# Optimization experiments

Measured on AMD Instinct MI355X. Metric: run time of the kernel, lower is better.

Reference implementation:

```python
import jax, jax.numpy as jnp
import numpy as np

C = 100000
D = 512
KEEP_RATIO = 0.5
EPS = 1.1920929e-07  # torch.finfo(float32).eps
K = max(1, int(C * KEEP_RATIO))


def _l2norm(x):
    # F.normalize(dim=-1): x / max(||x||, eps)
    n = jnp.linalg.norm(x, axis=-1, keepdims=True)
    return x / jnp.maximum(n, EPS)


def setup_inputs() -> dict:
    key = jax.random.key(0)
    k1, k2, k3 = jax.random.split(key, 3)
    tensor = jax.random.normal(k1, (1024, D), dtype=jnp.float32)
    target = jax.random.randint(k2, (1024,), 0, C, dtype=jnp.int32)
    # xavier_normal_ on (C, D): std = sqrt(2 / (C + D))
    std = np.sqrt(2.0 / (C + D)).astype(np.float32)
    weight = jax.random.normal(k3, (C, D), dtype=jnp.float32) * std
    return {"tensor": tensor, "target": target, "weight": weight}


def reference(tensor, target, weight):
    # --- target mining (no-grad in original) ---
    t_n = _l2norm(tensor)            # (B, D)
    w_n = _l2norm(weight)            # (C, D)
    # max over batch of cosine similarity -> per-class score (C,)
    scores = jnp.max(jnp.einsum("bd,cd->bc", t_n, w_n), axis=0)
    # ground-truth classes always kept
    scores = scores.at[target].set(2.0)
    _, topk_idx = jax.lax.top_k(scores, K)
    subsample = jnp.sort(topk_idx)                       # (K,) ascending
    # remap targets into subsampled index space (targets guaranteed present)
    new_target = jnp.searchsorted(subsample, target).astype(jnp.int32)
    # --- head ---
    w_sub = weight[subsample]                            # (K, D) gather
    logits = jnp.einsum("bd,kd->bk", _l2norm(tensor), _l2norm(w_sub))
    return logits, new_target
```

## Files before the change

### kernel.cpp

```cpp
#include <hip/hip_runtime.h>

#define C_CLS 100000
#define D_DIM 512
#define B_ROWS 1024
#define K_KEEP 50000
#define EPS_F 1.1920929e-07f
#define MB_CT 64
#define BAND 2e-3f
#define DELTA 4e-4f
#define RMAX 32768

typedef short v8s __attribute__((ext_vector_type(8)));
typedef float v4f __attribute__((ext_vector_type(4)));

struct Ctrl { unsigned prefix; unsigned need; };

__device__ __forceinline__ unsigned key_of(float f){
  unsigned u = __float_as_uint(f);
  return (u & 0x80000000u) ? ~u : (u | 0x80000000u);
}
__device__ __forceinline__ float key_inv(unsigned k){
  unsigned u = (k & 0x80000000u) ? (k & 0x7FFFFFFFu) : ~k;
  return __uint_as_float(u);
}
__device__ __forceinline__ unsigned short f2bf_rne(float f){
  unsigned u = __float_as_uint(f);
  unsigned r = (u + 0x7FFFu + ((u >> 16) & 1u)) >> 16;
  return (unsigned short)r;
}
__device__ __forceinline__ float bf2f(unsigned short h){
  return __uint_as_float(((unsigned)h) << 16);
}


__global__ __launch_bounds__(64) void norm_t_kernel(const float* __restrict__ t, float* __restrict__ tn,
                                                    unsigned short* __restrict__ tnph, unsigned short* __restrict__ tnpl,
                                                    const int* __restrict__ tgt, unsigned* __restrict__ keys){
  int row = blockIdx.x, lane = threadIdx.x;
  if (lane == 0) atomicMax(&keys[tgt[row]], key_of(2.0f));
  const float4* p = (const float4*)(t + (size_t)row * D_DIM);
  float4 a = p[lane*2+0], b = p[lane*2+1];
  float s = a.x*a.x + a.y*a.y + a.z*a.z + a.w*a.w
          + b.x*b.x + b.y*b.y + b.z*b.z + b.w*b.w;
  #pragma unroll
  for (int off = 32; off; off >>= 1) s += __shfl_xor(s, off);
  float den = fmaxf(sqrtf(s), EPS_F);
  float o[8] = {a.x/den, a.y/den, a.z/den, a.w/den, b.x/den, b.y/den, b.z/den, b.w/den};
  float4* q = (float4*)(tn + (size_t)row * D_DIM);
  q[lane*2+0] = make_float4(o[0],o[1],o[2],o[3]);
  q[lane*2+1] = make_float4(o[4],o[5],o[6],o[7]);
  v8s hv, lv;
  #pragma unroll
  for (int j = 0; j < 8; ++j){
    unsigned short h = f2bf_rne(o[j]);
    hv[j] = (short)h;
    lv[j] = (short)f2bf_rne(o[j] - bf2f(h));
  }
  size_t di = (size_t)((row & ~15) + (lane >> 2)) * 512 + (lane & 3) * 128 + (row & 15) * 8;
  *(v8s*)(tnph + di) = hv;
  *(v8s*)(tnpl + di) = lv;
}

__device__ __forceinline__ void load_a2(const unsigned short* __restrict__ tp, int b0, int ks, int lane, v8s* dst){
  #pragma unroll
  for (int i = 0; i < 2; ++i){
    int t = b0 + i*16 + (ks >> 5);
    dst[i] = *(const v8s*)(tp + (size_t)t * 512 + lane * 8);
  }
}

__global__ __launch_bounds__(512, 4) void mine_kernel(
    const unsigned short* __restrict__ tnph, const unsigned short* __restrict__ tnpl,
    const float* __restrict__ w, unsigned* __restrict__ keys,
    float* __restrict__ S, float* __restrict__ winv_g){
  __shared__ unsigned short lw[MB_CT * D_DIM];
  __shared__ float wn[MB_CT];
  const int tid = threadIdx.x;
  const int lane = tid & 63;
  const int cb = blockIdx.x * MB_CT;
  #pragma unroll
  for (int st = 0; st < 8; ++st){
    int g = tid + st * 512;
    int row = g >> 6, fc = g & 63;
    int c = cb + row; if (c >= C_CLS) c = C_CLS - 1;
    const float4* src = (const float4*)(w + (size_t)c * D_DIM + fc * 8);
    float4 v0 = src[0], v1 = src[1];
    float vv[8] = {v0.x,v0.y,v0.z,v0.w,v1.x,v1.y,v1.z,v1.w};
    float s = 0.f;
    #pragma unroll
    for (int j = 0; j < 8; ++j) s += vv[j]*vv[j];
    #pragma unroll
    for (int off = 32; off; off >>= 1) s += __shfl_xor(s, off);
    if (lane == 0) wn[row] = 1.0f / fmaxf(sqrtf(s), EPS_F);
    v8s hv;
    #pragma unroll
    for (int j = 0; j < 8; ++j) hv[j] = (short)f2bf_rne(vv[j]);
    int csw = fc ^ (row & 7);
    *(v8s*)&lw[(size_t)row * D_DIM + csw * 8] = hv;
  }
  __syncthreads();
  if (tid < MB_CT && cb + tid < C_CLS) winv_g[cb + tid] = wn[tid];

  const int wv = tid >> 6;
  const int lr = lane & 15, lg = lane >> 4;
  const int bbase = wv * 128;
  float runmax[4] = {-1e30f,-1e30f,-1e30f,-1e30f};
  v4f acc[4][2];
  #pragma unroll
  for (int j = 0; j < 4; ++j)
    #pragma unroll
    for (int i = 0; i < 2; ++i) acc[j][i] = (v4f){0.f,0.f,0.f,0.f};

  auto mfma_step = [&](int it, v8s* ah, v8s* al){
    const int ks = (it & 15) << 5;
    v8s bh[4];
    #pragma unroll
    for (int j = 0; j < 4; ++j){
      int row = j*16 + lr;
      int ch = ((ks >> 3) + lg) ^ (lr & 7);
      bh[j] = *(const v8s*)&lw[(size_t)row * D_DIM + ch * 8];
    }
    #pragma unroll
    for (int j = 0; j < 4; ++j)
      #pragma unroll
      for (int i = 0; i < 2; ++i){
        acc[j][i] = __builtin_amdgcn_mfma_f32_16x16x32_bf16(ah[i], bh[j], acc[j][i], 0, 0, 0);
        acc[j][i] = __builtin_amdgcn_mfma_f32_16x16x32_bf16(al[i], bh[j], acc[j][i], 0, 0, 0);
      }
  };
  auto flush = [&](int it){
    const int b0 = bbase + (it >> 4) * 32;
    #pragma unroll
    for (int j = 0; j < 4; ++j){
      float m = acc[j][0][0];
      #pragma unroll
      for (int i = 0; i < 2; ++i)
        #pragma unroll
        for (int r = 0; r < 4; ++r) m = fmaxf(m, acc[j][i][r]);
      runmax[j] = fmaxf(runmax[j], m);
      int cls = cb + j*16 + lr;
      if (cls < C_CLS){
        #pragma unroll
        for (int i = 0; i < 2; ++i){
          float4 v = make_float4(acc[j][i][0], acc[j][i][1], acc[j][i][2], acc[j][i][3]);
          *(float4*)(S + (size_t)cls * B_ROWS + b0 + i*16 + lg*4) = v;
        }
      }
      #pragma unroll
      for (int i = 0; i < 2; ++i) acc[j][i] = (v4f){0.f,0.f,0.f,0.f};
    }
  };

  v8s ah0[2], al0[2], ah1[2], al1[2];
  load_a2(tnph, bbase, 0, lane, ah0);
  load_a2(tnpl, bbase, 0, lane, al0);

  for (int it = 0; it < 64; it += 2){
    { int nit = it + 1;
      int nb0 = bbase + (nit >> 4) * 32, nks = (nit & 15) << 5;
      load_a2(tnph, nb0, nks, lane, ah1);
      load_a2(tnpl, nb0, nks, lane, al1); }
    mfma_step(it, ah0, al0);
    if (it + 2 < 64){
      int nit = it + 2;
      int nb0 = bbase + (nit >> 4) * 32, nks = (nit & 15) << 5;
      load_a2(tnph, nb0, nks, lane, ah0);
      load_a2(tnpl, nb0, nks, lane, al0); }
    mfma_step(it + 1, ah1, al1);
    if (((it + 1) & 15) == 15) flush(it + 1);
  }

  #pragma unroll
  for (int j = 0; j < 4; ++j){
    float m = runmax[j];
    m = fmaxf(m, __shfl_xor(m, 16));
    m = fmaxf(m, __shfl_xor(m, 32));
    int cls = cb + j*16 + lr;
    if (lg == 0 && cls < C_CLS)
      atomicMax(&keys[cls], key_of(m * wn[j*16 + lr]));
  }
}

__global__ __launch_bounds__(256) void histsel_kernel(const unsigned* __restrict__ keys, unsigned* __restrict__ hist,
                                                      unsigned* __restrict__ done, Ctrl* __restrict__ ctrl, int shift){
  __shared__ unsigned h[256];
  __shared__ int lastf;
  int t = threadIdx.x;
  h[t] = 0u;
  __syncthreads();
  unsigned himask = (shift >= 24) ? 0u : (0xFFFFFFFFu << (shift + 8));
  unsigned prefix = (shift == 24) ? 0u : (ctrl->prefix & himask);
  for (int c = blockIdx.x * 256 + t; c < C_CLS; c += gridDim.x * 256){
    unsigned k = keys[c];
    if ((k & himask) == prefix) atomicAdd(&h[(k >> shift) & 255], 1u);
  }
  __syncthreads();
  if (h[t]) atomicAdd(&hist[t], h[t]);
  __threadfence();
  if (t == 0) lastf = (atomicAdd(done, 1u) == (unsigned)(gridDim.x - 1));
  __syncthreads();
  if (lastf){
    unsigned v = __hip_atomic_load(&hist[t], __ATOMIC_RELAXED, __HIP_MEMORY_SCOPE_AGENT);
    h[t] = v;
    __syncthreads();
    if (t == 0){
      unsigned need = (shift == 24) ? (unsigned)K_KEEP : ctrl->need;
      unsigned pfx  = (shift == 24) ? 0u : ctrl->prefix;
      unsigned cum = 0; int b;
      for (b = 255; b >= 0; --b){
        if (cum + h[b] >= need) break;
        cum += h[b];
      }
      if (b < 0) b = 0;
      ctrl->prefix = pfx | ((unsigned)b << shift);
      ctrl->need = need - cum;
      __hip_atomic_store(done, 0u, __ATOMIC_RELAXED, __HIP_MEMORY_SCOPE_AGENT);
    }
    __hip_atomic_store(&hist[t], 0u, __ATOMIC_RELAXED, __HIP_MEMORY_SCOPE_AGENT);
  }
}

__global__ void band_kernel(const unsigned* __restrict__ keys, const Ctrl* __restrict__ ctrl,
                            int* __restrict__ rlist, int* __restrict__ rcount){
  int c = blockIdx.x * 256 + threadIdx.x;
  if (c >= C_CLS) return;
  unsigned k = keys[c];
  if (k == key_of(2.0f)) return;
  float t = key_inv(ctrl->prefix);
  if (fabsf(key_inv(k) - t) <= BAND){
    int i = atomicAdd(rcount, 1);
    if (i < RMAX) rlist[i] = c;
  }
}

__global__ __launch_bounds__(256) void refine_kernel(
    const float* __restrict__ tn, const float* __restrict__ w,
    const float* __restrict__ winv, const float* __restrict__ S,
    const int* __restrict__ rlist, const int* __restrict__ rcount,
    unsigned* __restrict__ keys){
  __shared__ float red[256];
  __shared__ double dred[256];
  __shared__ int cand[32];
  __shared__ int ncand;
  int n = *rcount; if (n > RMAX) n = RMAX;
  int t = threadIdx.x;
  for (int i = blockIdx.x; i < n; i += gridDim.x){
    int c = rlist[i];
    const v4f* srow = (const v4f*)(S + (size_t)c * B_ROWS);
    v4f sv = srow[t];
    float m = fmaxf(fmaxf(sv[0],sv[1]), fmaxf(sv[2],sv[3]));
    red[t] = m; __syncthreads();
    for (int off2 = 128; off2; off2 >>= 1){
      if (t < off2) red[t] = fmaxf(red[t], red[t+off2]);
      __syncthreads();
    }
    float thr = red[0] - DELTA;
    if (t == 0) ncand = 0;
    __syncthreads();
    #pragma unroll
    for (int e = 0; e < 4; ++e){
      if (sv[e] >= thr){
        int ci = atomicAdd(&ncand, 1);
        if (ci < 32) cand[ci] = t*4 + e;
      }
    }
    __syncthreads();
    int nc = ncand; if (nc > 32) nc = 32;
    const float* wrow = w + (size_t)c * D_DIM;
    double w0 = (double)wrow[2*t], w1 = (double)wrow[2*t+1];
    double best = -1e300;
    for (int q = 0; q < nc; ++q){
      int b = cand[q];
      const float* tr = tn + (size_t)b * D_DIM;
      double p = fma((double)tr[2*t], w0, (double)tr[2*t+1] * w1);
      dred[t] = p; __syncthreads();
      for (int off2 = 128; off2; off2 >>= 1){
        if (t < off2) dred[t] += dred[t+off2];
        __syncthreads();
      }
      if (t == 0) best = fmax(best, dred[0]);
      __syncthreads();
    }
    if (t == 0) keys[c] = key_of((float)(best * (double)winv[c]));
    __syncthreads();
  }
}

__global__ __launch_bounds__(256) void scanA_kernel(const unsigned* __restrict__ keys, const Ctrl* __restrict__ ctrl,
                                                    uint2* __restrict__ bsum2, unsigned* __restrict__ done2, int nb){
  __shared__ unsigned red[256];
  __shared__ int lastf;
  int t = threadIdx.x;
  unsigned T = ctrl->prefix;
  int base = blockIdx.x * 1024 + t * 4;
  unsigned pack = 0;
  #pragma unroll
  for (int j = 0; j < 4; ++j){
    int c = base + j;
    if (c < C_CLS){
      unsigned k = keys[c];
      if (k > T) pack += 0x10000u;
      else if (k == T) pack += 1u;
    }
  }
  red[t] = pack; __syncthreads();
  for (int off = 128; off; off >>= 1){
    if (t < off) red[t] += red[t + off];
    __syncthreads();
  }
  if (t == 0) bsum2[blockIdx.x] = make_uint2(red[0] >> 16, red[0] & 0xFFFFu);
  __threadfence();
  if (t == 0) lastf = (atomicAdd(done2, 1u) == (unsigned)(gridDim.x - 1));
  __syncthreads();
  if (lastf && t == 0){
    unsigned rg = 0, re = 0;
    for (int i = 0; i < nb; ++i){
      unsigned vx = __hip_atomic_load(&bsum2[i].x, __ATOMIC_RELAXED, __HIP_MEMORY_SCOPE_AGENT);
      unsigned vy = __hip_atomic_load(&bsum2[i].y, __ATOMIC_RELAXED, __HIP_MEMORY_SCOPE_AGENT);
      __hip_atomic_store(&bsum2[i].x, rg, __ATOMIC_RELAXED, __HIP_MEMORY_SCOPE_AGENT);
      __hip_atomic_store(&bsum2[i].y, re, __ATOMIC_RELAXED, __HIP_MEMORY_SCOPE_AGENT);
      rg += vx; re += vy;
    }
    __hip_atomic_store(done2, 0u, __ATOMIC_RELAXED, __HIP_MEMORY_SCOPE_AGENT);
  }
}

__global__ __launch_bounds__(256) void scanC_kernel(const unsigned* __restrict__ keys, const Ctrl* __restrict__ ctrl,
                                                    const uint2* __restrict__ bsum2, unsigned* __restrict__ pos,
                                                    int* __restrict__ sel){
  __shared__ unsigned ls[256];
  int t = threadIdx.x;
  unsigned T = ctrl->prefix, need = ctrl->need;
  int base = blockIdx.x * 1024 + t * 4;
  unsigned gtv[4], eqv[4], pack = 0;
  #pragma unroll
  for (int j = 0; j < 4; ++j){
    int c = base + j;
    unsigned k = (c < C_CLS) ? keys[c] : 0u;
    gtv[j] = (c < C_CLS && k > T) ? 1u : 0u;
    eqv[j] = (c < C_CLS && k == T) ? 1u : 0u;
    pack += (gtv[j] << 16) + eqv[j];
  }
  ls[t] = pack; __syncthreads();
  for (int off = 1; off < 256; off <<= 1){
    unsigned v = (t >= off) ? ls[t - off] : 0u;
    __syncthreads();
    ls[t] += v;
    __syncthreads();
  }
  unsigned excl = ls[t] - pack;
  uint2 bs = bsum2[blockIdx.x];
  unsigned gtx = bs.x + (excl >> 16);
  unsigned eqx = bs.y + (excl & 0xFFFFu);
  #pragma unroll
  for (int j = 0; j < 4; ++j){
    int c = base + j;
    if (c < C_CLS){
      unsigned p = gtx + (eqx < need ? eqx : need);
      pos[c] = p;
      if (gtv[j] || (eqv[j] && eqx < need)) sel[p] = c;
      gtx += gtv[j]; eqx += eqv[j];
    }
  }
}

__global__ void ntgt_kernel(const int* __restrict__ tgt, const unsigned* __restrict__ pos, float* __restrict__ out){
  int b = blockIdx.x * 256 + threadIdx.x;
  if (b < B_ROWS) out[(size_t)B_ROWS * K_KEEP + b] = (float)pos[tgt[b]];
}

__global__ __launch_bounds__(256) void head_copy_kernel(const float* __restrict__ S, const float* __restrict__ winv,
                                                        const int* __restrict__ sel, float* __restrict__ out){
  __shared__ float tile[64][68];
  __shared__ float wsc[64];
  int k0 = blockIdx.y * 64;
  int b0 = blockIdx.x * 64;
  int tid = threadIdx.x;
  int nk = K_KEEP - k0; if (nk > 64) nk = 64;
  if (tid < 64){
    int kk = k0 + tid;
    wsc[tid] = (kk < K_KEEP) ? winv[sel[kk]] : 0.f;
  }
  int r = tid >> 4, lq = tid & 15;
  #pragma unroll
  for (int itr = 0; itr < 4; ++itr){
    int i = itr * 16 + r;
    if (i < nk){
      int c = sel[k0 + i];
      float4 v = *(const float4*)(S + (size_t)c * B_ROWS + b0 + lq * 4);
      *(float4*)&tile[i][lq * 4] = v;
    }
  }
  __syncthreads();
  #pragma unroll
  for (int itw = 0; itw < 4; ++itw){
    int bb = itw * 16 + r;
    int kk = lq * 4;
    size_t obase = (size_t)(b0 + bb) * K_KEEP + k0;
    if (kk + 3 < nk){
      float4 v = make_float4(tile[kk+0][bb]*wsc[kk+0], tile[kk+1][bb]*wsc[kk+1],
                             tile[kk+2][bb]*wsc[kk+2], tile[kk+3][bb]*wsc[kk+3]);
      *(float4*)(out + obase + kk) = v;
    } else {
      for (int e = 0; e < 4; ++e)
        if (kk + e < nk) out[obase + kk + e] = tile[kk+e][bb]*wsc[kk+e];
    }
  }
}

extern "C" void kernel_launch(void* const* d_in, const int* in_sizes, int n_in,
                              void* d_out, int out_size, void* d_ws, size_t ws_size,
                              hipStream_t stream){
  const float* tensor = (const float*)d_in[0];
  const int*   target = (const int*)d_in[1];
  const float* weight = (const float*)d_in[2];
  float* out = (float*)d_out;

  char* ws = (char*)d_ws;
  size_t off = 0;
  auto carve = [&](size_t bytes) -> char* {
    char* p = ws + off;
    off = (off + bytes + 511) & ~(size_t)511;
    return p;
  };
  float*          tn   = (float*)carve((size_t)B_ROWS * D_DIM * 4);
  unsigned short* tnph = (unsigned short*)carve((size_t)B_ROWS * D_DIM * 2);
  unsigned short* tnpl = (unsigned short*)carve((size_t)B_ROWS * D_DIM * 2);
  float*          winv = (float*)carve((size_t)C_CLS * 4);
  size_t zs = off;
  unsigned* keys   = (unsigned*)carve((size_t)C_CLS * 4);
  unsigned* hist   = (unsigned*)carve(256 * 4);
  unsigned* done   = (unsigned*)carve(64);
  unsigned* done2  = (unsigned*)carve(64);
  int*      rcount = (int*)carve(64);
  size_t ze = off;
  Ctrl*     ctrl   = (Ctrl*)carve(64);
  uint2*    bsum2  = (uint2*)carve(128 * 8);
  int*      rlist  = (int*)carve((size_t)RMAX * 4);
  unsigned* pos    = (unsigned*)carve((size_t)C_CLS * 4);
  int*      sel    = (int*)carve((size_t)K_KEEP * 4);
  float*    S      = (float*)carve((size_t)C_CLS * B_ROWS * 4);
  (void)in_sizes; (void)n_in; (void)out_size; (void)ws_size;

  hipMemsetAsync(ws + zs, 0, ze - zs, stream);

  norm_t_kernel<<<B_ROWS, 64, 0, stream>>>(tensor, tn, tnph, tnpl, target, keys);

  mine_kernel<<<(C_CLS + MB_CT - 1) / MB_CT, 512, 0, stream>>>(tnph, tnpl, weight, keys, S, winv);

  for (int shift = 24; shift >= 0; shift -= 8)
    histsel_kernel<<<128, 256, 0, stream>>>(keys, hist, done, ctrl, shift);

  band_kernel<<<(C_CLS + 255) / 256, 256, 0, stream>>>(keys, ctrl, rlist, rcount);
  refine_kernel<<<2048, 256, 0, stream>>>(tn, weight, winv, S, rlist, rcount, keys);

  for (int shift = 24; shift >= 0; shift -= 8)
    histsel_kernel<<<128, 256, 0, stream>>>(keys, hist, done, ctrl, shift);

  const int nb = (C_CLS + 1023) / 1024;
  scanA_kernel<<<nb, 256, 0, stream>>>(keys, ctrl, bsum2, done2, nb);
  scanC_kernel<<<nb, 256, 0, stream>>>(keys, ctrl, bsum2, pos, sel);

  ntgt_kernel<<<(B_ROWS + 255) / 256, 256, 0, stream>>>(target, pos, out);
  head_copy_kernel<<<dim3(B_ROWS / 64, (K_KEEP + 63) / 64), 256, 0, stream>>>(S, winv, sel, out);
}
```

Baseline: 614.8 us.

## Double class tile per block to 128 with 1024 threads in mine kernel

The mining kernel now processes 128 classes per block with 1024 threads. Each wave covers 64 batch rows and all 8 class sub-tiles, so every A-fragment load is reused across twice as many B tiles. The explicit double-buffered A prefetch is dropped in favour of a simple per-iteration load. LDS use doubles to 128KB per block, and 16 accumulators per lane raise register pressure, which may cut occupancy and leave load latency less hidden.

```diff
diff --git a/kernel.cpp b/kernel.cpp
--- a/kernel.cpp
+++ b/kernel.cpp
@@ -5,7 +5,7 @@
 #define B_ROWS 1024
 #define K_KEEP 50000
 #define EPS_F 1.1920929e-07f
-#define MB_CT 64
+#define MB_CT 128
 #define BAND 2e-3f
 #define DELTA 4e-4f
 #define RMAX 32768
@@ -69,7 +69,7 @@
   }
 }
 
-__global__ __launch_bounds__(512, 4) void mine_kernel(
+__global__ __launch_bounds__(1024, 4) void mine_kernel(
     const unsigned short* __restrict__ tnph, const unsigned short* __restrict__ tnpl,
     const float* __restrict__ w, unsigned* __restrict__ keys,
     float* __restrict__ S, float* __restrict__ winv_g){
@@ -80,7 +80,7 @@
   const int cb = blockIdx.x * MB_CT;
   #pragma unroll
   for (int st = 0; st < 8; ++st){
-    int g = tid + st * 512;
+    int g = tid + st * 1024;
     int row = g >> 6, fc = g & 63;
     int c = cb + row; if (c >= C_CLS) c = C_CLS - 1;
     const float4* src = (const float4*)(w + (size_t)c * D_DIM + fc * 8);
@@ -103,75 +103,61 @@
 
   const int wv = tid >> 6;
   const int lr = lane & 15, lg = lane >> 4;
-  const int bbase = wv * 128;
-  float runmax[4] = {-1e30f,-1e30f,-1e30f,-1e30f};
-  v4f acc[4][2];
-  #pragma unroll
-  for (int j = 0; j < 4; ++j)
+  const int bbase = wv * 64;
+  float runmax[8] = {-1e30f,-1e30f,-1e30f,-1e30f,-1e30f,-1e30f,-1e30f,-1e30f};
+  v4f acc[8][2];
+  #pragma unroll
+  for (int j = 0; j < 8; ++j)
     #pragma unroll
     for (int i = 0; i < 2; ++i) acc[j][i] = (v4f){0.f,0.f,0.f,0.f};
 
-  auto mfma_step = [&](int it, v8s* ah, v8s* al){
-    const int ks = (it & 15) << 5;
-    v8s bh[4];
-    #pragma unroll
-    for (int j = 0; j < 4; ++j){
-      int row = j*16 + lr;
-      int ch = ((ks >> 3) + lg) ^ (lr & 7);
-      bh[j] = *(const v8s*)&lw[(size_t)row * D_DIM + ch * 8];
-    }
-    #pragma unroll
-    for (int j = 0; j < 4; ++j)
+  for (int it = 0; it < 32; ++it){
+    const int chunk = it >> 4, ks = (it & 15) << 5;
+    const int b0 = bbase + chunk * 32;
+    v8s cah[2], cal[2];
+    load_a2(tnph, b0, ks, lane, cah);
+    load_a2(tnpl, b0, ks, lane, cal);
+    #pragma unroll
+    for (int h = 0; h < 2; ++h){
+      v8s bh[4];
       #pragma unroll
-      for (int i = 0; i < 2; ++i){
-        acc[j][i] = __builtin_amdgcn_mfma_f32_16x16x32_bf16(ah[i], bh[j], acc[j][i], 0, 0, 0);
-        acc[j][i] = __builtin_amdgcn_mfma_f32_16x16x32_bf16(al[i], bh[j], acc[j][i], 0, 0, 0);
+      for (int j = 0; j < 4; ++j){
+        int row = (h*4 + j)*16 + lr;
+        int ch = ((ks >> 3) + lg) ^ (lr & 7);
+        bh[j] = *(const v8s*)&lw[(size_t)row * D_DIM + ch * 8];
       }
-  };
-  auto flush = [&](int it){
-    const int b0 = bbase + (it >> 4) * 32;
-    #pragma unroll
-    for (int j = 0; j < 4; ++j){
-      float m = acc[j][0][0];
       #pragma unroll
-      for (int i = 0; i < 2; ++i)
-        #pragma unroll
-        for (int r = 0; r < 4; ++r) m = fmaxf(m, acc[j][i][r]);
-      runmax[j] = fmaxf(runmax[j], m);
-      int cls = cb + j*16 + lr;
-      if (cls < C_CLS){
+      for (int j = 0; j < 4; ++j)
         #pragma unroll
         for (int i = 0; i < 2; ++i){
-          float4 v = make_float4(acc[j][i][0], acc[j][i][1], acc[j][i][2], acc[j][i][3]);
-          *(float4*)(S + (size_t)cls * B_ROWS + b0 + i*16 + lg*4) = v;
+          acc[h*4+j][i] = __builtin_amdgcn_mfma_f32_16x16x32_bf16(cah[i], bh[j], acc[h*4+j][i], 0, 0, 0);
+          acc[h*4+j][i] = __builtin_amdgcn_mfma_f32_16x16x32_bf16(cal[i], bh[j], acc[h*4+j][i], 0, 0, 0);
         }
+    }
+    if ((it & 15) == 15){
+      #pragma unroll
+      for (int j = 0; j < 8; ++j){
+        float m = acc[j][0][0];
+        #pragma unroll
+        for (int i = 0; i < 2; ++i)
+          #pragma unroll
+          for (int r = 0; r < 4; ++r) m = fmaxf(m, acc[j][i][r]);
+        runmax[j] = fmaxf(runmax[j], m);
+        int cls = cb + j*16 + lr;
+        if (cls < C_CLS){
+          #pragma unroll
+          for (int i = 0; i < 2; ++i){
+            float4 v = make_float4(acc[j][i][0], acc[j][i][1], acc[j][i][2], acc[j][i][3]);
+            *(float4*)(S + (size_t)cls * B_ROWS + b0 + i*16 + lg*4) = v;
+          }
+        }
+        #pragma unroll
+        for (int i = 0; i < 2; ++i) acc[j][i] = (v4f){0.f,0.f,0.f,0.f};
       }
-      #pragma unroll
-      for (int i = 0; i < 2; ++i) acc[j][i] = (v4f){0.f,0.f,0.f,0.f};
-    }
-  };
-
-  v8s ah0[2], al0[2], ah1[2], al1[2];
-  load_a2(tnph, bbase, 0, lane, ah0);
-  load_a2(tnpl, bbase, 0, lane, al0);
-
-  for (int it = 0; it < 64; it += 2){
-    { int nit = it + 1;
-      int nb0 = bbase + (nit >> 4) * 32, nks = (nit & 15) << 5;
-      load_a2(tnph, nb0, nks, lane, ah1);
-      load_a2(tnpl, nb0, nks, lane, al1); }
-    mfma_step(it, ah0, al0);
-    if (it + 2 < 64){
-      int nit = it + 2;
-      int nb0 = bbase + (nit >> 4) * 32, nks = (nit & 15) << 5;
-      load_a2(tnph, nb0, nks, lane, ah0);
-      load_a2(tnpl, nb0, nks, lane, al0); }
-    mfma_step(it + 1, ah1, al1);
-    if (((it + 1) & 15) == 15) flush(it + 1);
-  }
-
-  #pragma unroll
-  for (int j = 0; j < 4; ++j){
+    }
+  }
+  #pragma unroll
+  for (int j = 0; j < 8; ++j){
     float m = runmax[j];
     m = fmaxf(m, __shfl_xor(m, 16));
     m = fmaxf(m, __shfl_xor(m, 32));
@@ -446,7 +432,7 @@
 
   norm_t_kernel<<<B_ROWS, 64, 0, stream>>>(tensor, tn, tnph, tnpl, target, keys);
 
-  mine_kernel<<<(C_CLS + MB_CT - 1) / MB_CT, 512, 0, stream>>>(tnph, tnpl, weight, keys, S, winv);
+  mine_kernel<<<(C_CLS + MB_CT - 1) / MB_CT, 1024, 0, stream>>>(tnph, tnpl, weight, keys, S, winv);
 
   for (int shift = 24; shift >= 0; shift -= 8)
     histsel_kernel<<<128, 256, 0, stream>>>(keys, hist, done, ctrl, shift);
```

After: 626.3 us. About the same (+1.9%).

## Stream A-operand tiles through LDS via async global_load_lds double buffering

Applied to the files above, without the earlier changes.

Replaces the register-prefetched A-operand loads in the mining kernel with async global-to-LDS copies into a per-wave double buffer, waiting on vmcnt before reading each stage from LDS. The aim is to free VGPRs and overlap global-memory latency with the MFMA work. It doubles the kernel's shared-memory footprint and lowers the launch-bounds occupancy hint from 4 blocks to 1, which may cut resident waves available to hide latency.

```diff
diff --git a/kernel.cpp b/kernel.cpp
--- a/kernel.cpp
+++ b/kernel.cpp
@@ -31,6 +31,10 @@
 __device__ __forceinline__ float bf2f(unsigned short h){
   return __uint_as_float(((unsigned)h) << 16);
 }
+__device__ __forceinline__ void gload_lds16(const unsigned short* g, unsigned short* l){
+  __builtin_amdgcn_global_load_lds((const __attribute__((address_space(1))) unsigned int*)g,
+                                   (__attribute__((address_space(3))) unsigned int*)l, 16, 0, 0);
+}
 
 
 __global__ __launch_bounds__(64) void norm_t_kernel(const float* __restrict__ t, float* __restrict__ tn,
@@ -61,19 +65,12 @@
   *(v8s*)(tnpl + di) = lv;
 }
 
-__device__ __forceinline__ void load_a2(const unsigned short* __restrict__ tp, int b0, int ks, int lane, v8s* dst){
-  #pragma unroll
-  for (int i = 0; i < 2; ++i){
-    int t = b0 + i*16 + (ks >> 5);
-    dst[i] = *(const v8s*)(tp + (size_t)t * 512 + lane * 8);
-  }
-}
-
-__global__ __launch_bounds__(512, 4) void mine_kernel(
+__global__ __launch_bounds__(512, 1) void mine_kernel(
     const unsigned short* __restrict__ tnph, const unsigned short* __restrict__ tnpl,
     const float* __restrict__ w, unsigned* __restrict__ keys,
     float* __restrict__ S, float* __restrict__ winv_g){
   __shared__ unsigned short lw[MB_CT * D_DIM];
+  __shared__ unsigned short lA[8 * 4096];
   __shared__ float wn[MB_CT];
   const int tid = threadIdx.x;
   const int lane = tid & 63;
@@ -104,6 +101,7 @@
   const int wv = tid >> 6;
   const int lr = lane & 15, lg = lane >> 4;
   const int bbase = wv * 128;
+  unsigned short* aw = lA + wv * 4096;
   float runmax[4] = {-1e30f,-1e30f,-1e30f,-1e30f};
   v4f acc[4][2];
   #pragma unroll
@@ -111,7 +109,35 @@
     #pragma unroll
     for (int i = 0; i < 2; ++i) acc[j][i] = (v4f){0.f,0.f,0.f,0.f};
 
-  auto mfma_step = [&](int it, v8s* ah, v8s* al){
+  auto issueA = [&](int buf, int it){
+    const int b0 = bbase + (it >> 4) * 32;
+    const int kt = it & 15;
+    unsigned short* dst = aw + buf * 2048;
+    #pragma unroll
+    for (int i = 0; i < 2; ++i){
+      int t = b0 + i * 16 + kt;
+      gload_lds16(tnph + (size_t)t * 512 + lane * 8, dst + i * 512);
+      gload_lds16(tnpl + (size_t)t * 512 + lane * 8, dst + 1024 + i * 512);
+    }
+  };
+
+  issueA(0, 0);
+  for (int it = 0; it < 64; ++it){
+    const int buf = it & 1;
+    if (it < 63){
+      issueA(buf ^ 1, it + 1);
+      asm volatile("s_waitcnt vmcnt(4)" ::: "memory");
+    } else {
+      asm volatile("s_waitcnt vmcnt(0)" ::: "memory");
+    }
+    __builtin_amdgcn_sched_barrier(0);
+    const unsigned short* src = aw + buf * 2048;
+    v8s ah[2], al[2];
+    #pragma unroll
+    for (int i = 0; i < 2; ++i){
+      ah[i] = *(const v8s*)(src + i * 512 + lane * 8);
+      al[i] = *(const v8s*)(src + 1024 + i * 512 + lane * 8);
+    }
     const int ks = (it & 15) << 5;
     v8s bh[4];
     #pragma unroll
@@ -127,49 +153,29 @@
         acc[j][i] = __builtin_amdgcn_mfma_f32_16x16x32_bf16(ah[i], bh[j], acc[j][i], 0, 0, 0);
         acc[j][i] = __builtin_amdgcn_mfma_f32_16x16x32_bf16(al[i], bh[j], acc[j][i], 0, 0, 0);
       }
-  };
-  auto flush = [&](int it){
-    const int b0 = bbase + (it >> 4) * 32;
-    #pragma unroll
-    for (int j = 0; j < 4; ++j){
-      float m = acc[j][0][0];
+    if ((it & 15) == 15){
+      const int b0 = bbase + (it >> 4) * 32;
       #pragma unroll
-      for (int i = 0; i < 2; ++i)
+      for (int j = 0; j < 4; ++j){
+        float m = acc[j][0][0];
         #pragma unroll
-        for (int r = 0; r < 4; ++r) m = fmaxf(m, acc[j][i][r]);
-      runmax[j] = fmaxf(runmax[j], m);
-      int cls = cb + j*16 + lr;
-      if (cls < C_CLS){
+        for (int i = 0; i < 2; ++i)
+          #pragma unroll
+          for (int r = 0; r < 4; ++r) m = fmaxf(m, acc[j][i][r]);
+        runmax[j] = fmaxf(runmax[j], m);
+        int cls = cb + j*16 + lr;
+        if (cls < C_CLS){
+          #pragma unroll
+          for (int i = 0; i < 2; ++i){
+            float4 v = make_float4(acc[j][i][0], acc[j][i][1], acc[j][i][2], acc[j][i][3]);
+            *(float4*)(S + (size_t)cls * B_ROWS + b0 + i*16 + lg*4) = v;
+          }
+        }
         #pragma unroll
-        for (int i = 0; i < 2; ++i){
-          float4 v = make_float4(acc[j][i][0], acc[j][i][1], acc[j][i][2], acc[j][i][3]);
-          *(float4*)(S + (size_t)cls * B_ROWS + b0 + i*16 + lg*4) = v;
-        }
+        for (int i = 0; i < 2; ++i) acc[j][i] = (v4f){0.f,0.f,0.f,0.f};
       }
-      #pragma unroll
-      for (int i = 0; i < 2; ++i) acc[j][i] = (v4f){0.f,0.f,0.f,0.f};
-    }
-  };
-
-  v8s ah0[2], al0[2], ah1[2], al1[2];
-  load_a2(tnph, bbase, 0, lane, ah0);
-  load_a2(tnpl, bbase, 0, lane, al0);
-
-  for (int it = 0; it < 64; it += 2){
-    { int nit = it + 1;
-      int nb0 = bbase + (nit >> 4) * 32, nks = (nit & 15) << 5;
-      load_a2(tnph, nb0, nks, lane, ah1);
-      load_a2(tnpl, nb0, nks, lane, al1); }
-    mfma_step(it, ah0, al0);
-    if (it + 2 < 64){
-      int nit = it + 2;
-      int nb0 = bbase + (nit >> 4) * 32, nks = (nit & 15) << 5;
-      load_a2(tnph, nb0, nks, lane, ah0);
-      load_a2(tnpl, nb0, nks, lane, al0); }
-    mfma_step(it + 1, ah1, al1);
-    if (((it + 1) & 15) == 15) flush(it + 1);
-  }
-
+    }
+  }
   #pragma unroll
   for (int j = 0; j < 4; ++j){
     float m = runmax[j];
```

New measurement: 710.5 us. +15.6%, slower.
